# Performance work log

Measured on AMD Instinct MI355X. Metric: run time of the kernel, lower is better.

## Reference

```python
import jax, jax.numpy as jnp
import numpy as np

B, S, H = 16, 2048, 1024
N_SEG = 512  # number of extracted number-vectors (loop runs i in [0, n))


def setup_inputs() -> dict:
    key = jax.random.key(0)
    k_in, = jax.random.split(key, 1)
    inp = jax.random.normal(k_in, (B, S, H), dtype=jnp.float32)
    # number_mask values in [0, N_SEG]; max value == N_SEG so torch's
    # n = max(number_mask) == N_SEG and ids 0..N_SEG-1 all occur.
    number_mask = (jnp.arange(B * S, dtype=jnp.int64) % (N_SEG + 1)).reshape(B, S)
    return {"input": inp, "number_mask": number_mask, "n": N_SEG, "concat": 1}


def reference(input, number_mask, n, concat):
    # Flatten to row-major order, matching torch.nonzero's (batch, seq) ordering.
    L = input.shape[0] * input.shape[1]
    x_flat = input.reshape(L, input.shape[2])          # [B*S, H]
    ids = number_mask.reshape(L)                        # [B*S]
    pos = jnp.arange(L, dtype=jnp.int32)
    # First/last row-major occurrence of each segment id i in [0, n).
    # Ids >= n (i.e. == max) are dropped by segment_* (out-of-range), exactly
    # as the original loop never visits i == n.
    first_idx = jax.ops.segment_min(pos, ids, num_segments=n)  # [n]
    last_idx = jax.ops.segment_max(pos, ids, num_segments=n)   # [n]
    first = x_flat[first_idx]                           # [n, H]
    last = x_flat[last_idx]                             # [n, H]
    if concat:
        return jnp.concatenate((first, last), axis=-1)  # [n, 2H]
    return first + last                                  # [n, H]
```

## Files before the change

kernel.cpp:

```cpp
#include <hip/hip_runtime.h>

__global__ void scan_minmax(const int* __restrict__ mask, int L, int n,
                            int* __restrict__ first, int* __restrict__ last) {
    extern __shared__ int smem[];
    int* s_first = smem;
    int* s_last  = smem + n;
    for (int i = threadIdx.x; i < n; i += blockDim.x) {
        s_first[i] = 0x7fffffff;
        s_last[i]  = -1;
    }
    __syncthreads();
    for (int pos = threadIdx.x; pos < L; pos += blockDim.x) {
        int id = mask[pos];
        if (id >= 0 && id < n) {
            atomicMin(&s_first[id], pos);
            atomicMax(&s_last[id], pos);
        }
    }
    __syncthreads();
    for (int i = threadIdx.x; i < n; i += blockDim.x) {
        first[i] = s_first[i];
        last[i]  = s_last[i];
    }
}

__global__ void gather_rows(const float4* __restrict__ x,
                            const int* __restrict__ first,
                            const int* __restrict__ last,
                            float4* __restrict__ out, int H4) {
    int i = blockIdx.x;
    int f = first[i];
    int l = last[i];
    const float4* __restrict__ sf = x + (size_t)f * H4;
    const float4* __restrict__ sl = x + (size_t)l * H4;
    float4* __restrict__ dst = out + (size_t)i * (size_t)(2 * H4);
    for (int t = threadIdx.x; t < H4; t += blockDim.x) {
        dst[t]      = sf[t];
        dst[H4 + t] = sl[t];
    }
}

extern "C" void kernel_launch(void* const* d_in, const int* in_sizes, int n_in,
                              void* d_out, int out_size, void* d_ws, size_t ws_size,
                              hipStream_t stream) {
    const float* x  = (const float*)d_in[0];
    const int* mask = (const int*)d_in[1];

    const int L = in_sizes[1];
    const int H = in_sizes[0] / L;
    const int n = out_size / (2 * H);

    int* first = (int*)d_ws;
    int* last  = first + n;

    scan_minmax<<<1, 1024, 2 * n * sizeof(int), stream>>>(mask, L, n, first, last);

    const int H4 = H / 4;
    gather_rows<<<n, 256, 0, stream>>>((const float4*)x, first, last,
                                       (float4*)d_out, H4);
}
```

Measured before the change: 181.2 us.

## Fuse segment min/max scan into gather with one block per segment

Replaces the single-block atomic scan plus separate gather kernel with one kernel in which each of n blocks scans the whole mask (as int4 vector loads) for its own segment id, reduces min/max with wave shuffles and shared memory, then copies the two rows. This removes the serial single-block bottleneck, the shared-memory atomic contention and one kernel launch. In exchange the mask is read n times (mostly from cache), and L is assumed divisible by 4. Segments that never occur fall back to row 0 instead of an out-of-range index.

```diff
diff --git a/kernel.cpp b/kernel.cpp
--- a/kernel.cpp
+++ b/kernel.cpp
@@ -1,42 +1,45 @@
 #include <hip/hip_runtime.h>
 
-__global__ void scan_minmax(const int* __restrict__ mask, int L, int n,
-                            int* __restrict__ first, int* __restrict__ last) {
-    extern __shared__ int smem[];
-    int* s_first = smem;
-    int* s_last  = smem + n;
-    for (int i = threadIdx.x; i < n; i += blockDim.x) {
-        s_first[i] = 0x7fffffff;
-        s_last[i]  = -1;
+__global__ __launch_bounds__(1024) void fused_seg_gather(
+    const int4* __restrict__ mask4, const float4* __restrict__ x,
+    float4* __restrict__ out, int L4, int H4) {
+    const int seg = blockIdx.x;
+
+    int fmin = 0x7fffffff;
+    int fmax = -1;
+    for (int k = threadIdx.x; k < L4; k += blockDim.x) {
+        int4 m = mask4[k];
+        int base = k << 2;
+        if (m.x == seg) { fmin = min(fmin, base);     fmax = max(fmax, base);     }
+        if (m.y == seg) { fmin = min(fmin, base + 1); fmax = max(fmax, base + 1); }
+        if (m.z == seg) { fmin = min(fmin, base + 2); fmax = max(fmax, base + 2); }
+        if (m.w == seg) { fmin = min(fmin, base + 3); fmax = max(fmax, base + 3); }
+    }
+
+    for (int off = 32; off > 0; off >>= 1) {
+        fmin = min(fmin, __shfl_down(fmin, off, 64));
+        fmax = max(fmax, __shfl_down(fmax, off, 64));
+    }
+    __shared__ int s_min[16], s_max[16];
+    const int wave = threadIdx.x >> 6;
+    if ((threadIdx.x & 63) == 0) { s_min[wave] = fmin; s_max[wave] = fmax; }
+    __syncthreads();
+    const int nwaves = blockDim.x >> 6;
+    if (threadIdx.x == 0) {
+        int m = s_min[0], M = s_max[0];
+        for (int w = 1; w < nwaves; ++w) { m = min(m, s_min[w]); M = max(M, s_max[w]); }
+        s_min[0] = m; s_max[0] = M;
     }
     __syncthreads();
-    for (int pos = threadIdx.x; pos < L; pos += blockDim.x) {
-        int id = mask[pos];
-        if (id >= 0 && id < n) {
-            atomicMin(&s_first[id], pos);
-            atomicMax(&s_last[id], pos);
-        }
-    }
-    __syncthreads();
-    for (int i = threadIdx.x; i < n; i += blockDim.x) {
-        first[i] = s_first[i];
-        last[i]  = s_last[i];
-    }
-}
+    int f = s_min[0];
+    int l = s_max[0];
+    if (l < 0) { f = 0; l = 0; }
 
-__global__ void gather_rows(const float4* __restrict__ x,
-                            const int* __restrict__ first,
-                            const int* __restrict__ last,
-                            float4* __restrict__ out, int H4) {
-    int i = blockIdx.x;
-    int f = first[i];
-    int l = last[i];
     const float4* __restrict__ sf = x + (size_t)f * H4;
     const float4* __restrict__ sl = x + (size_t)l * H4;
-    float4* __restrict__ dst = out + (size_t)i * (size_t)(2 * H4);
-    for (int t = threadIdx.x; t < H4; t += blockDim.x) {
-        dst[t]      = sf[t];
-        dst[H4 + t] = sl[t];
+    float4* __restrict__ dst = out + (size_t)seg * (size_t)(2 * H4);
+    for (int t = threadIdx.x; t < 2 * H4; t += blockDim.x) {
+        dst[t] = (t < H4) ? sf[t] : sl[t - H4];
     }
 }
 
@@ -50,12 +53,9 @@
     const int H = in_sizes[0] / L;
     const int n = out_size / (2 * H);
 
-    int* first = (int*)d_ws;
-    int* last  = first + n;
+    const int L4 = L / 4;
+    const int H4 = H / 4;
 
-    scan_minmax<<<1, 1024, 2 * n * sizeof(int), stream>>>(mask, L, n, first, last);
-
-    const int H4 = H / 4;
-    gather_rows<<<n, 256, 0, stream>>>((const float4*)x, first, last,
-                                       (float4*)d_out, H4);
+    fused_seg_gather<<<n, 1024, 0, stream>>>((const int4*)mask, (const float4*)x,
+                                             (float4*)d_out, L4, H4);
 }
```

After: 167.9 us. 7.4% less time.
